# Kernel tuning notes

Measured on AMD Instinct MI355X. Metric: run time of the kernel, lower is better.

The kernel has to match this reference:

```python
import jax, jax.numpy as jnp
import numpy as np

ALPHA = 0.2  # LeakyReLU negative slope (module init arg)


def setup_inputs() -> dict:
    key = jax.random.key(0)
    ks = jax.random.split(key, 5)
    b, w, K, E = 8, 256, 256, 512  # batch, window_size, n_features, embed (=2*window)
    x = jax.random.normal(ks[0], (b, w, K), dtype=jnp.float32)
    W = jax.random.normal(ks[1], (E, 2 * w), dtype=jnp.float32) * 0.05
    b_lin = jax.random.normal(ks[2], (E,), dtype=jnp.float32) * 0.05
    a = jax.random.normal(ks[3], (E,), dtype=jnp.float32) * 0.05
    bias = jax.random.normal(ks[4], (K, K), dtype=jnp.float32) * 0.05
    return {"x": x, "W": W, "b_lin": b_lin, "a": a, "bias": bias}


def reference(x, W, b_lin, a, bias):
    # x: (b, window, K) -> v: (b, K, window)
    v = jnp.transpose(x, (0, 2, 1))
    w = v.shape[2]
    # lin(concat(v_i, v_j)) == v_i @ Wl^T + v_j @ Wr^T + b_lin  (split weight)
    Wl, Wr = W[:, :w], W[:, w:]
    left = jnp.einsum('bkw,ew->bke', v, Wl)    # (b, K, E)
    right = jnp.einsum('bkw,ew->bke', v, Wr)   # (b, K, E)
    pre = left[:, :, None, :] + right[:, None, :, :] + b_lin  # (b, K, K, E)
    act = jax.nn.leaky_relu(pre, negative_slope=ALPHA)
    e = jnp.einsum('bije,e->bij', act, a) + bias               # (b, K, K)
    attn = jax.nn.softmax(e, axis=2)  # dropout p=0 in eval -> identity
    h = jax.nn.sigmoid(jnp.einsum('bij,bjw->biw', attn, v))    # (b, K, window)
    return jnp.transpose(h, (0, 2, 1))                          # (b, window, K)
```

## Files before the change

kernel.cpp:

```cpp
#include <hip/hip_runtime.h>
#include <math.h>

typedef float f32x4 __attribute__((ext_vector_type(4)));
typedef __bf16 bf16x8 __attribute__((ext_vector_type(8)));
typedef unsigned short u16x8 __attribute__((ext_vector_type(8)));

__device__ __forceinline__ unsigned short f2bf(float f) {
    union { float f; unsigned int u; } v; v.f = f;
    unsigned int u = v.u;
    return (unsigned short)((u + 0x7fffu + ((u >> 16) & 1u)) >> 16);
}
__device__ __forceinline__ float bf_lo(unsigned int d) {
    union { unsigned int u; float f; } v; v.u = d << 16; return v.f;
}
__device__ __forceinline__ float bf_hi(unsigned int d) {
    union { unsigned int u; float f; } v; v.u = d & 0xffff0000u; return v.f;
}
__device__ __forceinline__ float sigmoidf_(float v) {
    return 1.f / (1.f + __expf(-v));
}

__global__ __launch_bounds__(256) void mfma_gemm_kernel(
    const float* __restrict__ x,
    const float* __restrict__ W,
    const float* __restrict__ b_lin,
    float* __restrict__ Lp,
    unsigned short* __restrict__ R2)
{
    const int b = blockIdx.y;
    const int t = blockIdx.x;
    const bool left = (t < 32);
    int m0, n0;
    if (left) { m0 = (t >> 3) * 64; n0 = (t & 7) * 64; }
    else      { const int tt = t - 32; m0 = (tt >> 2) * 64; n0 = (tt & 3) * 64; }

    __shared__ unsigned short As[64][72];
    __shared__ unsigned short Bs[64][72];

    unsigned short (*Ts)[72] = left ? As : Bs;
    unsigned short (*Ds)[72] = left ? Bs : As;
    const int cbase = left ? m0 : n0;
    const int rbase = left ? n0 : m0;
    const int coff  = left ? 0 : 256;

    const int tid  = threadIdx.x;
    const int wv   = tid >> 6;
    const int lane = tid & 63;
    const int wy = wv >> 1, wx = wv & 1;
    const int lr = lane & 15;
    const int lk = lane >> 4;

    const float* xb = x + b * 65536;

    f32x4 acc[2][2];
    #pragma unroll
    for (int i = 0; i < 2; i++)
        #pragma unroll
        for (int jj = 0; jj < 2; jj++) acc[i][jj] = (f32x4){0.f, 0.f, 0.f, 0.f};

    const int wl = tid >> 4;
    const int kg = tid & 15;
    const int dr = tid >> 2;
    const int dc = (tid & 3) * 16;

    for (int k0 = 0; k0 < 256; k0 += 64) {
        #pragma unroll
        for (int p = 0; p < 4; p++) {
            const int w = wl + 16 * p;
            const float4 v = *(const float4*)(xb + (k0 + w) * 256 + cbase + kg * 4);
            Ts[kg * 4 + 0][w] = f2bf(v.x);
            Ts[kg * 4 + 1][w] = f2bf(v.y);
            Ts[kg * 4 + 2][w] = f2bf(v.z);
            Ts[kg * 4 + 3][w] = f2bf(v.w);
        }
        {
            const float* src = W + (rbase + dr) * 512 + coff + k0 + dc;
            const float4 v0 = *(const float4*)(src);
            const float4 v1 = *(const float4*)(src + 4);
            const float4 v2 = *(const float4*)(src + 8);
            const float4 v3 = *(const float4*)(src + 12);
            u16x8 o0, o1;
            o0[0] = f2bf(v0.x); o0[1] = f2bf(v0.y); o0[2] = f2bf(v0.z); o0[3] = f2bf(v0.w);
            o0[4] = f2bf(v1.x); o0[5] = f2bf(v1.y); o0[6] = f2bf(v1.z); o0[7] = f2bf(v1.w);
            o1[0] = f2bf(v2.x); o1[1] = f2bf(v2.y); o1[2] = f2bf(v2.z); o1[3] = f2bf(v2.w);
            o1[4] = f2bf(v3.x); o1[5] = f2bf(v3.y); o1[6] = f2bf(v3.z); o1[7] = f2bf(v3.w);
            *(u16x8*)&Ds[dr][dc]     = o0;
            *(u16x8*)&Ds[dr][dc + 8] = o1;
        }
        __syncthreads();
        #pragma unroll
        for (int kk = 0; kk < 64; kk += 32) {
            const bf16x8 a0 = *(const bf16x8*)&As[wy * 32 + lr][kk + lk * 8];
            const bf16x8 a1 = *(const bf16x8*)&As[wy * 32 + 16 + lr][kk + lk * 8];
            const bf16x8 b0 = *(const bf16x8*)&Bs[wx * 32 + lr][kk + lk * 8];
            const bf16x8 b1 = *(const bf16x8*)&Bs[wx * 32 + 16 + lr][kk + lk * 8];
            acc[0][0] = __builtin_amdgcn_mfma_f32_16x16x32_bf16(a0, b0, acc[0][0], 0, 0, 0);
            acc[0][1] = __builtin_amdgcn_mfma_f32_16x16x32_bf16(a0, b1, acc[0][1], 0, 0, 0);
            acc[1][0] = __builtin_amdgcn_mfma_f32_16x16x32_bf16(a1, b0, acc[1][0], 0, 0, 0);
            acc[1][1] = __builtin_amdgcn_mfma_f32_16x16x32_bf16(a1, b1, acc[1][1], 0, 0, 0);
        }
        __syncthreads();
    }

    if (left) {
        #pragma unroll
        for (int mi = 0; mi < 2; mi++) {
            #pragma unroll
            for (int ni = 0; ni < 2; ni++) {
                const int row = m0 + wy * 32 + mi * 16 + lk * 4;
                const int col = n0 + wx * 32 + ni * 16 + lr;
                const float bl = b_lin[col];
                #pragma unroll
                for (int r = 0; r < 4; r++)
                    Lp[b * 131072 + (row + r) * 512 + col] = acc[mi][ni][r] + bl;
            }
        }
    } else {
        unsigned short* R2b = R2 + b * 131072;
        #pragma unroll
        for (int mi = 0; mi < 2; mi++) {
            #pragma unroll
            for (int ni = 0; ni < 2; ni++) {
                const int row = m0 + wy * 32 + mi * 16 + lk * 4;
                const int col = n0 + wx * 32 + ni * 16 + lr;
                ushort4 o;
                o.x = f2bf(acc[mi][ni][0]);
                o.y = f2bf(acc[mi][ni][1]);
                o.z = f2bf(acc[mi][ni][2]);
                o.w = f2bf(acc[mi][ni][3]);
                *(ushort4*)(R2b + (row >> 3) * 2048 + col * 8 + (row & 7)) = o;
            }
        }
    }
}

__global__ __launch_bounds__(512, 8) void attn_kernel(
    const float* __restrict__ x,
    const float* __restrict__ Lp,
    const unsigned int* __restrict__ R2u,
    const float* __restrict__ a,
    const float* __restrict__ bias,
    float* __restrict__ out)
{
    const int b   = blockIdx.x & 7;
    const int i0  = (blockIdx.x >> 3) * 4;
    const int tid = threadIdx.x;
    const int j   = tid & 255;
    const int eh  = tid >> 8;

    __shared__ float Lt[512][4];
    __shared__ float aS[512];
    __shared__ float acc2P[2][4][256];
    __shared__ float rgp[2][256];
    __shared__ float u15s[4];
    __shared__ unsigned short atbf[16 * 264];

    {
        const int i  = tid >> 7;
        const int e0 = (tid & 127) * 4;
        const float4 v = *(const float4*)(Lp + b * 131072 + (i0 + i) * 512 + e0);
        Lt[e0 + 0][i] = v.x;
        Lt[e0 + 1][i] = v.y;
        Lt[e0 + 2][i] = v.z;
        Lt[e0 + 3][i] = v.w;
        aS[tid] = a[tid];
    }

    if (tid < 256) {
        const int i = tid >> 6, lane = tid & 63;
        const float* Lr = Lp + b * 131072 + (i0 + i) * 512 + lane * 8;
        const float* ar = a + lane * 8;
        const float4 la = *(const float4*)Lr;
        const float4 lb = *(const float4*)(Lr + 4);
        const float4 ca = *(const float4*)ar;
        const float4 cb = *(const float4*)(ar + 4);
        float p = la.x * ca.x + la.y * ca.y + la.z * ca.z + la.w * ca.w
                + lb.x * cb.x + lb.y * cb.y + lb.z * cb.z + lb.w * cb.w;
        #pragma unroll
        for (int off = 32; off; off >>= 1) p += __shfl_xor(p, off);
        if (lane == 0) u15s[i] = 0.6f * p;
    }
    __syncthreads();

    const float* aq = aS + eh * 256;
    const float (*Ltq)[4] = (const float (*)[4])(Lt + eh * 256);
    const uint4* Rq = (const uint4*)(R2u + b * 65536) + (eh * 32) * 256 + j;

    float acc0 = 0.f, acc1 = 0.f, acc2 = 0.f, acc3 = 0.f, rsum = 0.f;

    uint4 cur = Rq[0];
    for (int tk = 0; tk < 32; tk++) {
        uint4 nxt;
        if (tk < 31) nxt = Rq[(tk + 1) * 256];
        float r[8];
        r[0] = bf_lo(cur.x); r[1] = bf_hi(cur.x);
        r[2] = bf_lo(cur.y); r[3] = bf_hi(cur.y);
        r[4] = bf_lo(cur.z); r[5] = bf_hi(cur.z);
        r[6] = bf_lo(cur.w); r[7] = bf_hi(cur.w);
        #pragma unroll
        for (int q2 = 0; q2 < 2; q2++) {
            const float4 av4 = *(const float4*)&aq[tk * 8 + q2 * 4];
            #pragma unroll
            for (int s = 0; s < 4; s++) {
                const int e = tk * 8 + q2 * 4 + s;
                const float4 lv = *(const float4*)Ltq[e];
                const float ae = ((const float*)&av4)[s];
                const float rv = r[q2 * 4 + s];
                rsum = fmaf(ae, rv, rsum);
                acc0 = fmaf(ae, fabsf(lv.x + rv), acc0);
                acc1 = fmaf(ae, fabsf(lv.y + rv), acc1);
                acc2 = fmaf(ae, fabsf(lv.z + rv), acc2);
                acc3 = fmaf(ae, fabsf(lv.w + rv), acc3);
            }
        }
        cur = nxt;
    }
    acc2P[eh][0][j] = acc0;
    acc2P[eh][1][j] = acc1;
    acc2P[eh][2][j] = acc2;
    acc2P[eh][3][j] = acc3;
    rgp[eh][j] = rsum;
    __syncthreads();

    if (tid < 256) {
        const int i = tid >> 6, lane = tid & 63;
        const float u15 = u15s[i];
        float v[4];
        float m = -1e30f;
        #pragma unroll
        for (int u = 0; u < 4; u++) {
            const int jj = lane + 64 * u;
            const float uR = rgp[0][jj] + rgp[1][jj];
            const float ab = acc2P[0][i][jj] + acc2P[1][i][jj];
            v[u] = u15 + 0.6f * uR + 0.4f * ab + bias[(i0 + i) * 256 + jj];
            m = fmaxf(m, v[u]);
        }
        #pragma unroll
        for (int off = 32; off; off >>= 1) m = fmaxf(m, __shfl_xor(m, off));
        float s = 0.f;
        #pragma unroll
        for (int u = 0; u < 4; u++) { v[u] = __expf(v[u] - m); s += v[u]; }
        #pragma unroll
        for (int off = 32; off; off >>= 1) s += __shfl_xor(s, off);
        const float inv = 1.f / s;
        #pragma unroll
        for (int u = 0; u < 4; u++)
            atbf[i * 264 + lane + 64 * u] = f2bf(v[u] * inv);
    }
    __syncthreads();

    {
        const int wvv  = tid >> 6;
        const int lane = tid & 63;
        const int lr = lane & 15;
        const int lk = lane >> 4;
        #pragma unroll
        for (int half = 0; half < 2; half++) {
            const int nt = wvv + half * 8;
            f32x4 hacc = (f32x4){0.f, 0.f, 0.f, 0.f};
            const float* xw = x + b * 65536 + (nt * 16 + lr) * 256;
            #pragma unroll
            for (int kt = 0; kt < 8; kt++) {
                const bf16x8 av = *(const bf16x8*)&atbf[lr * 264 + kt * 32 + lk * 8];
                const float4 f0 = *(const float4*)(xw + kt * 32 + lk * 8);
                const float4 f1 = *(const float4*)(xw + kt * 32 + lk * 8 + 4);
                u16x8 bu;
                bu[0] = f2bf(f0.x); bu[1] = f2bf(f0.y); bu[2] = f2bf(f0.z); bu[3] = f2bf(f0.w);
                bu[4] = f2bf(f1.x); bu[5] = f2bf(f1.y); bu[6] = f2bf(f1.z); bu[7] = f2bf(f1.w);
                const bf16x8 bv = *(const bf16x8*)&bu;
                hacc = __builtin_amdgcn_mfma_f32_16x16x32_bf16(av, bv, hacc, 0, 0, 0);
            }
            if (lk == 0) {
                float4 o;
                o.x = sigmoidf_(hacc[0]);
                o.y = sigmoidf_(hacc[1]);
                o.z = sigmoidf_(hacc[2]);
                o.w = sigmoidf_(hacc[3]);
                *(float4*)(out + b * 65536 + (nt * 16 + lr) * 256 + i0) = o;
            }
        }
    }
}

extern "C" void kernel_launch(void* const* d_in, const int* in_sizes, int n_in,
                              void* d_out, int out_size, void* d_ws, size_t ws_size,
                              hipStream_t stream) {
    const float* x     = (const float*)d_in[0];
    const float* W     = (const float*)d_in[1];
    const float* b_lin = (const float*)d_in[2];
    const float* a     = (const float*)d_in[3];
    const float* bias  = (const float*)d_in[4];
    float* out = (float*)d_out;

    char* ws = (char*)d_ws;
    float*          Lp = (float*)ws;
    unsigned short* R2 = (unsigned short*)(ws + (4 << 20));

    mfma_gemm_kernel<<<dim3(64, 8), 256, 0, stream>>>(x, W, b_lin, Lp, R2);
    attn_kernel<<<512, 512, 0, stream>>>(x, Lp, (const unsigned int*)R2, a, bias, out);
}
```

Baseline: 107.8 us.

## Register-tile attn scores: each thread handles 4 j columns across 8 e-slices

The attention score loop is re-partitioned: each wave now owns a 64-wide slice of the embedding dimension and each lane computes a 4x4 (i,j) register tile, instead of one j per thread over half of E. This reuses each LDS-loaded L vector and a coefficient across four j values, cutting shared-memory reads per FMA. In exchange the partial sums must be reduced across 8 slices through a larger shared buffer, and the launch-bounds occupancy hint drops from 8 to 4 to allow more registers, which may reduce latency hiding.

Measured after the change: 164.9 us. 1.53x slower.

```diff
diff --git a/kernel.cpp b/kernel.cpp
--- a/kernel.cpp
+++ b/kernel.cpp
@@ -134,7 +134,7 @@
     }
 }
 
-__global__ __launch_bounds__(512, 8) void attn_kernel(
+__global__ __launch_bounds__(512, 4) void attn_kernel(
     const float* __restrict__ x,
     const float* __restrict__ Lp,
     const unsigned int* __restrict__ R2u,
@@ -142,16 +142,16 @@
     const float* __restrict__ bias,
     float* __restrict__ out)
 {
-    const int b   = blockIdx.x & 7;
-    const int i0  = (blockIdx.x >> 3) * 4;
-    const int tid = threadIdx.x;
-    const int j   = tid & 255;
-    const int eh  = tid >> 8;
+    const int b    = blockIdx.x & 7;
+    const int i0   = (blockIdx.x >> 3) * 4;
+    const int tid  = threadIdx.x;
+    const int wv   = tid >> 6;
+    const int lane = tid & 63;
 
     __shared__ float Lt[512][4];
     __shared__ float aS[512];
-    __shared__ float acc2P[2][4][256];
-    __shared__ float rgp[2][256];
+    __shared__ float acc2P[8][4][256];
+    __shared__ float rgp[8][256];
     __shared__ float u15s[4];
     __shared__ unsigned short atbf[16 * 264];
 
@@ -167,9 +167,9 @@
     }
 
     if (tid < 256) {
-        const int i = tid >> 6, lane = tid & 63;
-        const float* Lr = Lp + b * 131072 + (i0 + i) * 512 + lane * 8;
-        const float* ar = a + lane * 8;
+        const int i = tid >> 6, ln = tid & 63;
+        const float* Lr = Lp + b * 131072 + (i0 + i) * 512 + ln * 8;
+        const float* ar = a + ln * 8;
         const float4 la = *(const float4*)Lr;
         const float4 lb = *(const float4*)(Lr + 4);
         const float4 ca = *(const float4*)ar;
@@ -178,60 +178,78 @@
                 + lb.x * cb.x + lb.y * cb.y + lb.z * cb.z + lb.w * cb.w;
         #pragma unroll
         for (int off = 32; off; off >>= 1) p += __shfl_xor(p, off);
-        if (lane == 0) u15s[i] = 0.6f * p;
+        if (ln == 0) u15s[i] = 0.6f * p;
     }
     __syncthreads();
 
-    const float* aq = aS + eh * 256;
-    const float (*Ltq)[4] = (const float (*)[4])(Lt + eh * 256);
-    const uint4* Rq = (const uint4*)(R2u + b * 65536) + (eh * 32) * 256 + j;
-
-    float acc0 = 0.f, acc1 = 0.f, acc2 = 0.f, acc3 = 0.f, rsum = 0.f;
-
-    uint4 cur = Rq[0];
-    for (int tk = 0; tk < 32; tk++) {
-        uint4 nxt;
-        if (tk < 31) nxt = Rq[(tk + 1) * 256];
-        float r[8];
-        r[0] = bf_lo(cur.x); r[1] = bf_hi(cur.x);
-        r[2] = bf_lo(cur.y); r[3] = bf_hi(cur.y);
-        r[4] = bf_lo(cur.z); r[5] = bf_hi(cur.z);
-        r[6] = bf_lo(cur.w); r[7] = bf_hi(cur.w);
-        #pragma unroll
-        for (int q2 = 0; q2 < 2; q2++) {
-            const float4 av4 = *(const float4*)&aq[tk * 8 + q2 * 4];
-            #pragma unroll
-            for (int s = 0; s < 4; s++) {
-                const int e = tk * 8 + q2 * 4 + s;
-                const float4 lv = *(const float4*)Ltq[e];
-                const float ae = ((const float*)&av4)[s];
-                const float rv = r[q2 * 4 + s];
-                rsum = fmaf(ae, rv, rsum);
-                acc0 = fmaf(ae, fabsf(lv.x + rv), acc0);
-                acc1 = fmaf(ae, fabsf(lv.y + rv), acc1);
-                acc2 = fmaf(ae, fabsf(lv.z + rv), acc2);
-                acc3 = fmaf(ae, fabsf(lv.w + rv), acc3);
-            }
-        }
-        cur = nxt;
-    }
-    acc2P[eh][0][j] = acc0;
-    acc2P[eh][1][j] = acc1;
-    acc2P[eh][2][j] = acc2;
-    acc2P[eh][3][j] = acc3;
-    rgp[eh][j] = rsum;
+    const float* aq = aS + wv * 64;
+    const float (*Ltq)[4] = (const float (*)[4])(Lt + wv * 64);
+    const uint4* Rq = (const uint4*)(R2u + b * 65536) + (wv * 8) * 256 + lane * 4;
+
+    float acc[4][4];
+    #pragma unroll
+    for (int i = 0; i < 4; i++)
+        #pragma unroll
+        for (int jj = 0; jj < 4; jj++) acc[i][jj] = 0.f;
+    float rsum[4] = {0.f, 0.f, 0.f, 0.f};
+
+    #pragma unroll
+    for (int tk = 0; tk < 8; tk++) {
+        const uint4 rw0 = Rq[tk * 256 + 0];
+        const uint4 rw1 = Rq[tk * 256 + 1];
+        const uint4 rw2 = Rq[tk * 256 + 2];
+        const uint4 rw3 = Rq[tk * 256 + 3];
+        float r[4][8];
+        r[0][0]=bf_lo(rw0.x); r[0][1]=bf_hi(rw0.x); r[0][2]=bf_lo(rw0.y); r[0][3]=bf_hi(rw0.y);
+        r[0][4]=bf_lo(rw0.z); r[0][5]=bf_hi(rw0.z); r[0][6]=bf_lo(rw0.w); r[0][7]=bf_hi(rw0.w);
+        r[1][0]=bf_lo(rw1.x); r[1][1]=bf_hi(rw1.x); r[1][2]=bf_lo(rw1.y); r[1][3]=bf_hi(rw1.y);
+        r[1][4]=bf_lo(rw1.z); r[1][5]=bf_hi(rw1.z); r[1][6]=bf_lo(rw1.w); r[1][7]=bf_hi(rw1.w);
+        r[2][0]=bf_lo(rw2.x); r[2][1]=bf_hi(rw2.x); r[2][2]=bf_lo(rw2.y); r[2][3]=bf_hi(rw2.y);
+        r[2][4]=bf_lo(rw2.z); r[2][5]=bf_hi(rw2.z); r[2][6]=bf_lo(rw2.w); r[2][7]=bf_hi(rw2.w);
+        r[3][0]=bf_lo(rw3.x); r[3][1]=bf_hi(rw3.x); r[3][2]=bf_lo(rw3.y); r[3][3]=bf_hi(rw3.y);
+        r[3][4]=bf_lo(rw3.z); r[3][5]=bf_hi(rw3.z); r[3][6]=bf_lo(rw3.w); r[3][7]=bf_hi(rw3.w);
+
+        const float4 av0 = *(const float4*)&aq[tk * 8];
+        const float4 av1 = *(const float4*)&aq[tk * 8 + 4];
+        #pragma unroll
+        for (int s = 0; s < 8; s++) {
+            const float4 lv = *(const float4*)Ltq[tk * 8 + s];
+            const float ae = (s < 4) ? ((const float*)&av0)[s]
+                                     : ((const float*)&av1)[s - 4];
+            #pragma unroll
+            for (int jj = 0; jj < 4; jj++) {
+                const float rv = r[jj][s];
+                rsum[jj] = fmaf(ae, rv, rsum[jj]);
+                acc[0][jj] = fmaf(ae, fabsf(lv.x + rv), acc[0][jj]);
+                acc[1][jj] = fmaf(ae, fabsf(lv.y + rv), acc[1][jj]);
+                acc[2][jj] = fmaf(ae, fabsf(lv.z + rv), acc[2][jj]);
+                acc[3][jj] = fmaf(ae, fabsf(lv.w + rv), acc[3][jj]);
+            }
+        }
+    }
+    #pragma unroll
+    for (int i = 0; i < 4; i++)
+        #pragma unroll
+        for (int jj = 0; jj < 4; jj++)
+            acc2P[wv][i][lane * 4 + jj] = acc[i][jj];
+    #pragma unroll
+    for (int jj = 0; jj < 4; jj++) rgp[wv][lane * 4 + jj] = rsum[jj];
     __syncthreads();
 
     if (tid < 256) {
-        const int i = tid >> 6, lane = tid & 63;
+        const int i = tid >> 6, ln = tid & 63;
         const float u15 = u15s[i];
         float v[4];
         float m = -1e30f;
         #pragma unroll
         for (int u = 0; u < 4; u++) {
-            const int jj = lane + 64 * u;
-            const float uR = rgp[0][jj] + rgp[1][jj];
-            const float ab = acc2P[0][i][jj] + acc2P[1][i][jj];
+            const int jj = ln + 64 * u;
+            float uR = 0.f, ab = 0.f;
+            #pragma unroll
+            for (int eo = 0; eo < 8; eo++) {
+                uR += rgp[eo][jj];
+                ab += acc2P[eo][i][jj];
+            }
             v[u] = u15 + 0.6f * uR + 0.4f * ab + bias[(i0 + i) * 256 + jj];
             m = fmaxf(m, v[u]);
         }
@@ -245,18 +263,16 @@
         const float inv = 1.f / s;
         #pragma unroll
         for (int u = 0; u < 4; u++)
-            atbf[i * 264 + lane + 64 * u] = f2bf(v[u] * inv);
+            atbf[i * 264 + ln + 64 * u] = f2bf(v[u] * inv);
     }
     __syncthreads();
 
     {
-        const int wvv  = tid >> 6;
-        const int lane = tid & 63;
         const int lr = lane & 15;
         const int lk = lane >> 4;
         #pragma unroll
         for (int half = 0; half < 2; half++) {
-            const int nt = wvv + half * 8;
+            const int nt = wv + half * 8;
             f32x4 hacc = (f32x4){0.f, 0.f, 0.f, 0.f};
             const float* xw = x + b * 65536 + (nt * 16 + lr) * 256;
             #pragma unroll
```
